# Kernel optimization log

Hardware: AMD Instinct MI355X
Metric: run time of the kernel (lower is better)

Reference implementation:

```python
import jax, jax.numpy as jnp
import numpy as np

B = 262144
HIST = 24
FORE = 20
HID = 256
# torch: tau_int = clamp(tau,1,18).long().item(); default tau=6.0 -> static 6 (host sync in torch)
TAU_INT = 6


def setup_inputs() -> dict:
    key = jax.random.key(0)
    ks = jax.random.split(key, 9)
    s = 0.1
    return {
        "history": jax.random.normal(ks[0], (B, HIST), jnp.float32),
        "enc_w1": jax.random.normal(ks[1], (HIST + FORE, HID), jnp.float32) * s,
        "enc_b1": jnp.zeros((HID,), jnp.float32),
        "enc_w2": jax.random.normal(ks[2], (HID, HID), jnp.float32) * s,
        "enc_b2": jnp.zeros((HID,), jnp.float32),
        "cor_w1": jax.random.normal(ks[3], (HID, HID), jnp.float32) * s,
        "cor_b1": jnp.zeros((HID,), jnp.float32),
        "cor_w2": jax.random.normal(ks[4], (HID, FORE), jnp.float32) * s,
        "cor_b2": jnp.zeros((FORE,), jnp.float32),
        "alpha": jnp.float32(0.2),
        "beta": jnp.float32(0.3),
        "gamma": jnp.float32(0.01),
        "tau": jnp.float32(6.0),
        "lambda_mix": jnp.float32(0.5),
    }


def _physics_core(history, alpha, beta, gamma, steps):
    a = jax.nn.sigmoid(alpha)
    b = jax.nn.sigmoid(beta)
    g = jnp.abs(gamma)
    T0 = history[:, -1]                      # [B]
    buf0 = history[:, -TAU_INT:].T           # [tau, B]; buf0[0] = history[:, -tau]

    def step(carry, _):
        T, buf = carry
        T_delayed = buf[0]
        T_new = T - a * T - b * T_delayed - g * T ** 3
        buf = jnp.concatenate([buf[1:], T_new[None, :]], axis=0)
        return (T_new, buf), T_new

    _, preds = jax.lax.scan(step, (T0, buf0), None, length=steps)
    return preds.T                            # [B, steps]


def reference(history, enc_w1, enc_b1, enc_w2, enc_b2,
              cor_w1, cor_b1, cor_w2, cor_b2,
              alpha, beta, gamma, tau, lambda_mix):
    T_physics = _physics_core(history, alpha, beta, gamma, FORE)   # [B, FORE]
    combined = jnp.concatenate([history, T_physics], axis=1)       # [B, HIST+FORE]
    h = jnp.tanh(combined @ enc_w1 + enc_b1)
    features = jnp.tanh(h @ enc_w2 + enc_b2)
    c = jnp.tanh(features @ cor_w1 + cor_b1)
    T_soft = c @ cor_w2 + cor_b2                                   # [B, FORE]
    lam = jax.nn.sigmoid(lambda_mix)
    T_pred = T_physics + lam * T_soft
    return (T_pred, T_physics, T_soft)
```

## Files before the change

### kernel.cpp

```cpp
#include <hip/hip_runtime.h>
#include <hip/hip_bf16.h>

#define NROWS 262144
#define HISTC 24
#define FOREC 20

typedef __bf16        v8bf __attribute__((ext_vector_type(8)));
typedef float         v4f  __attribute__((ext_vector_type(4)));
typedef float         v2f  __attribute__((ext_vector_type(2)));
typedef unsigned int  v4u  __attribute__((ext_vector_type(4)));
typedef unsigned int  v2u  __attribute__((ext_vector_type(2)));

#define WS_WT1_OFF 64
#define WT1_ELEMS 16384
#define WT2_ELEMS 65536
#define WT3_ELEMS 65536
#define WT4_ELEMS 8192

__device__ __forceinline__ unsigned short f2bf(float x) {
    unsigned u = __builtin_bit_cast(unsigned, x);
    u += 0x7FFFu + ((u >> 16) & 1u);
    return (unsigned short)(u >> 16);
}

__device__ __forceinline__ unsigned pack2bf(float a, float b) {
    unsigned ua = __builtin_bit_cast(unsigned, a);
    unsigned ub = __builtin_bit_cast(unsigned, b);
    ua += 0x7FFFu + ((ua >> 16) & 1u);
    ub += 0x7FFFu + ((ub >> 16) & 1u);
    return (ua >> 16) | (ub & 0xFFFF0000u);
}

__device__ __forceinline__ float fast_tanh(float x) {
    float t = x * 2.885390081777927f;
    float p = __builtin_amdgcn_exp2f(t);
    float r = __builtin_amdgcn_rcpf(p + 1.0f);
    return __builtin_fmaf(-2.0f, r, 1.0f);
}

__global__ void prep_kernel(const float* __restrict__ w1, const float* __restrict__ w2,
                            const float* __restrict__ w3, const float* __restrict__ w4,
                            const float* __restrict__ alpha, const float* __restrict__ beta,
                            const float* __restrict__ gamma, const float* __restrict__ lmix,
                            unsigned char* __restrict__ ws)
{
    if (blockIdx.x == 76) {
        int t = threadIdx.x;
        float* wsf = (float*)ws;
        if (t == 0) wsf[0] = 1.0f / (1.0f + expf(-alpha[0]));
        else if (t == 1) wsf[1] = 1.0f / (1.0f + expf(-beta[0]));
        else if (t == 2) wsf[2] = fabsf(gamma[0]);
        else if (t == 3) wsf[3] = 1.0f / (1.0f + expf(-lmix[0]));
        return;
    }
    int idx = (blockIdx.x * 256 + threadIdx.x) * 8;
    const float* src;
    int KT, Kreal, Nreal, srcN, local;
    unsigned short* dst = (unsigned short*)(ws + WS_WT1_OFF);
    if (idx < WT1_ELEMS) {
        local = idx; src = w1; KT = 2; Kreal = 44; Nreal = 256; srcN = 256;
    } else if (idx < WT1_ELEMS + WT2_ELEMS) {
        local = idx - WT1_ELEMS; dst += WT1_ELEMS;
        src = w2; KT = 8; Kreal = 256; Nreal = 256; srcN = 256;
    } else if (idx < WT1_ELEMS + WT2_ELEMS + WT3_ELEMS) {
        local = idx - (WT1_ELEMS + WT2_ELEMS); dst += WT1_ELEMS + WT2_ELEMS;
        src = w3; KT = 8; Kreal = 256; Nreal = 256; srcN = 256;
    } else {
        local = idx - (WT1_ELEMS + WT2_ELEMS + WT3_ELEMS);
        dst += WT1_ELEMS + WT2_ELEMS + WT3_ELEMS;
        src = w4; KT = 8; Kreal = 256; Nreal = 20; srcN = 20;
    }
    int L   = (local >> 3) & 63;
    int blk = local >> 9;
    int kt = blk % KT, nt = blk / KT;
    int cc = L & 15,  qq = L >> 4;
    int feat = nt * 16 + cc;
    int kbase = kt * 32 + qq * 8;
    unsigned short tmp[8];
#pragma unroll
    for (int j = 0; j < 8; ++j) {
        int k = kbase + j;
        float v = (k < Kreal && feat < Nreal) ? src[k * srcN + feat] : 0.0f;
        tmp[j] = f2bf(v);
    }
    v4u pk;
    pk[0] = tmp[0] | ((unsigned)tmp[1] << 16);
    pk[1] = tmp[2] | ((unsigned)tmp[3] << 16);
    pk[2] = tmp[4] | ((unsigned)tmp[5] << 16);
    pk[3] = tmp[6] | ((unsigned)tmp[7] << 16);
    *(v4u*)&dst[local] = pk;
}

template<int KT>
__device__ __forceinline__ void layer123(unsigned short* buf,
        const unsigned short* __restrict__ wsw, const float* __restrict__ bias,
        int w, int c, int q, int lane)
{
    const v4u* wp = (const v4u*)wsw;
    v4f acc[4][4];
#pragma unroll
    for (int ft = 0; ft < 4; ++ft)
#pragma unroll
        for (int st = 0; st < 4; ++st) {
            v4f z = {0.0f, 0.0f, 0.0f, 0.0f};
            acc[ft][st] = z;
        }

#pragma unroll 2
    for (int kt = 0; kt < KT; ++kt) {
        v4u a[4];
#pragma unroll
        for (int ft = 0; ft < 4; ++ft)
            a[ft] = wp[((w * 4 + ft) * KT + kt) * 64 + lane];
#pragma unroll
        for (int st = 0; st < 4; ++st) {
            v4u braw = *(const v4u*)&buf[(st * 16 + c) * 264 + kt * 32 + q * 8];
            v8bf bb = __builtin_bit_cast(v8bf, braw);
#pragma unroll
            for (int ft = 0; ft < 4; ++ft)
                acc[ft][st] = __builtin_amdgcn_mfma_f32_16x16x32_bf16(
                    __builtin_bit_cast(v8bf, a[ft]), bb, acc[ft][st], 0, 0, 0);
        }
    }

    __syncthreads();

#pragma unroll
    for (int ft = 0; ft < 4; ++ft) {
        v4f bi = *(const v4f*)&bias[w * 64 + ft * 16 + q * 4];
#pragma unroll
        for (int st = 0; st < 4; ++st) {
            float x0 = fast_tanh(acc[ft][st][0] + bi[0]);
            float x1 = fast_tanh(acc[ft][st][1] + bi[1]);
            float x2 = fast_tanh(acc[ft][st][2] + bi[2]);
            float x3 = fast_tanh(acc[ft][st][3] + bi[3]);
            v2u d; d[0] = pack2bf(x0, x1); d[1] = pack2bf(x2, x3);
            *(v2u*)&buf[(st * 16 + c) * 264 + w * 64 + ft * 16 + q * 4] = d;
        }
    }
    __syncthreads();
}

__global__ __launch_bounds__(256, 4) void fused_kernel(
    const float* __restrict__ history,
    const float* __restrict__ eb1, const float* __restrict__ eb2,
    const float* __restrict__ cb1, const float* __restrict__ cb2,
    const unsigned char* __restrict__ ws, float* __restrict__ out)
{
    __shared__ unsigned short buf[64 * 264];
    __shared__ float tp[64 * 20];

    const int tid  = threadIdx.x;
    const int w    = tid >> 6;
    const int lane = tid & 63;
    const int c    = lane & 15;
    const int q    = lane >> 4;
    const int row0 = blockIdx.x << 6;
    const float* wsf = (const float*)ws;
    const unsigned short* wt1 = (const unsigned short*)(ws + WS_WT1_OFF);
    const unsigned short* wt2 = wt1 + WT1_ELEMS;
    const unsigned short* wt3 = wt2 + WT2_ELEMS;
    const unsigned short* wt4 = wt3 + WT3_ELEMS;

#pragma unroll
    for (int i = 0; i < 2; ++i) {
        int e = tid + i * 256;
        if (e < 384) {
            int r  = e / 6, c4 = e - r * 6;
            v4f h4 = *(const v4f*)&history[(long)(row0 + r) * 24 + c4 * 4];
            v2u d; d[0] = pack2bf(h4[0], h4[1]); d[1] = pack2bf(h4[2], h4[3]);
            *(v2u*)&buf[r * 264 + c4 * 4] = d;
        }
    }
#pragma unroll
    for (int i = 0; i < 2; ++i) {
        int e = tid + i * 256;
        if (e < 320) {
            int r = e / 5, g = e - r * 5;
            v2u z = {0u, 0u};
            *(v2u*)&buf[r * 264 + 44 + g * 4] = z;
        }
    }
    if (tid < 64) {
        const float* hrow = &history[(long)(row0 + tid) * 24];
        v2f h18 = *(const v2f*)&hrow[18];
        v4f h20 = *(const v4f*)&hrow[20];
        float pa = wsf[0], pb = wsf[1], pg = wsf[2];
        float d0 = h18[0], d1 = h18[1], d2 = h20[0];
        float d3 = h20[1], d4 = h20[2], d5 = h20[3];
        float T = d5;
#pragma unroll
        for (int s = 0; s < 20; ++s) {
            float t3 = T * T * T;
            float Tn = T - pa * T;
            Tn = Tn - pb * d0;
            Tn = Tn - pg * t3;
            tp[tid * 20 + s] = Tn;
            buf[tid * 264 + 24 + s] = f2bf(Tn);
            d0 = d1; d1 = d2; d2 = d3; d3 = d4; d4 = d5; d5 = Tn;
            T = Tn;
        }
    }
    __syncthreads();

    layer123<2>(buf, wt1, eb1, w, c, q, lane);
    layer123<8>(buf, wt2, eb2, w, c, q, lane);
    layer123<8>(buf, wt3, cb1, w, c, q, lane);

    const v4u* wp4 = (const v4u*)wt4;
    v4f acc40 = {0.0f, 0.0f, 0.0f, 0.0f}, acc41 = {0.0f, 0.0f, 0.0f, 0.0f};
#pragma unroll 2
    for (int kt = 0; kt < 8; ++kt) {
        v4u a0 = wp4[(0 * 8 + kt) * 64 + lane];
        v4u a1 = wp4[(1 * 8 + kt) * 64 + lane];
        v4u braw = *(const v4u*)&buf[(w * 16 + c) * 264 + kt * 32 + q * 8];
        v8bf bb = __builtin_bit_cast(v8bf, braw);
        acc40 = __builtin_amdgcn_mfma_f32_16x16x32_bf16(
            __builtin_bit_cast(v8bf, a0), bb, acc40, 0, 0, 0);
        acc41 = __builtin_amdgcn_mfma_f32_16x16x32_bf16(
            __builtin_bit_cast(v8bf, a1), bb, acc41, 0, 0, 0);
    }

    const float lam = wsf[3];
    const long sample = (long)row0 + w * 16 + c;
    float* outP = out;
    float* outF = out + (long)NROWS * 20;
    float* outS = out + (long)NROWS * 40;
    {
        int f0 = q * 4;
        v4f bi  = *(const v4f*)&cb2[f0];
        v4f tph = *(const v4f*)&tp[(w * 16 + c) * 20 + f0];
        v4f ts, pr;
#pragma unroll
        for (int r = 0; r < 4; ++r) {
            ts[r] = acc40[r] + bi[r];
            pr[r] = tph[r] + lam * ts[r];
        }
        *(v4f*)&outS[sample * 20 + f0] = ts;
        *(v4f*)&outP[sample * 20 + f0] = pr;
        *(v4f*)&outF[sample * 20 + f0] = tph;
    }
    if (q == 0) {
        v4f bi  = *(const v4f*)&cb2[16];
        v4f tph = *(const v4f*)&tp[(w * 16 + c) * 20 + 16];
        v4f ts, pr;
#pragma unroll
        for (int r = 0; r < 4; ++r) {
            ts[r] = acc41[r] + bi[r];
            pr[r] = tph[r] + lam * ts[r];
        }
        *(v4f*)&outS[sample * 20 + 16] = ts;
        *(v4f*)&outP[sample * 20 + 16] = pr;
        *(v4f*)&outF[sample * 20 + 16] = tph;
    }
}

extern "C" void kernel_launch(void* const* d_in, const int* in_sizes, int n_in,
                              void* d_out, int out_size, void* d_ws, size_t ws_size,
                              hipStream_t stream)
{
    const float* history = (const float*)d_in[0];
    const float* enc_w1  = (const float*)d_in[1];
    const float* enc_b1  = (const float*)d_in[2];
    const float* enc_w2  = (const float*)d_in[3];
    const float* enc_b2  = (const float*)d_in[4];
    const float* cor_w1  = (const float*)d_in[5];
    const float* cor_b1  = (const float*)d_in[6];
    const float* cor_w2  = (const float*)d_in[7];
    const float* cor_b2  = (const float*)d_in[8];
    const float* alpha   = (const float*)d_in[9];
    const float* beta    = (const float*)d_in[10];
    const float* gamma   = (const float*)d_in[11];
    const float* lmix    = (const float*)d_in[13];

    prep_kernel<<<77, 256, 0, stream>>>(enc_w1, enc_w2, cor_w1, cor_w2,
                                        alpha, beta, gamma, lmix,
                                        (unsigned char*)d_ws);
    fused_kernel<<<NROWS / 64, 256, 0, stream>>>(history, enc_b1, enc_b2, cor_b1, cor_b2,
                                                 (const unsigned char*)d_ws, (float*)d_out);
}
```

Measured before the change: 210.9 us.

## Software-pipeline weight fragment loads across layers with a three-slot register ring

Replaces per-k-step weight loads with a triple-buffered register ring that prefetches weight fragments two k-steps ahead. The prefetch carries across layer boundaries, so the next layer's first tiles load during the current one. The last layer's weights are replicated per wave (the workspace grows), which lets each wave index its own copy in the prefetch. Launch bounds drop from 4 to 3 blocks per CU to make room for the extra registers, at the cost of occupancy.

```diff
diff --git a/kernel.cpp b/kernel.cpp
--- a/kernel.cpp
+++ b/kernel.cpp
@@ -15,7 +15,7 @@
 #define WT1_ELEMS 16384
 #define WT2_ELEMS 65536
 #define WT3_ELEMS 65536
-#define WT4_ELEMS 8192
+#define WT4R_ELEMS 65536
 
 __device__ __forceinline__ unsigned short f2bf(float x) {
     unsigned u = __builtin_bit_cast(unsigned, x);
@@ -23,7 +23,7 @@
     return (unsigned short)(u >> 16);
 }
 
-__device__ __forceinline__ unsigned pack2bf(float a, float b) {
+__device__ __forceinline__ unsigned packbf2(float a, float b) {
     unsigned ua = __builtin_bit_cast(unsigned, a);
     unsigned ub = __builtin_bit_cast(unsigned, b);
     ua += 0x7FFFu + ((ua >> 16) & 1u);
@@ -44,7 +44,7 @@
                             const float* __restrict__ gamma, const float* __restrict__ lmix,
                             unsigned char* __restrict__ ws)
 {
-    if (blockIdx.x == 76) {
+    if (blockIdx.x == 104) {
         int t = threadIdx.x;
         float* wsf = (float*)ws;
         if (t == 0) wsf[0] = 1.0f / (1.0f + expf(-alpha[0]));
@@ -55,24 +55,24 @@
     }
     int idx = (blockIdx.x * 256 + threadIdx.x) * 8;
     const float* src;
-    int KT, Kreal, Nreal, srcN, local;
+    int KT, Kreal, Nreal, srcN, local, ntmask;
     unsigned short* dst = (unsigned short*)(ws + WS_WT1_OFF);
     if (idx < WT1_ELEMS) {
-        local = idx; src = w1; KT = 2; Kreal = 44; Nreal = 256; srcN = 256;
+        local = idx; src = w1; KT = 2; Kreal = 44; Nreal = 256; srcN = 256; ntmask = 255;
     } else if (idx < WT1_ELEMS + WT2_ELEMS) {
         local = idx - WT1_ELEMS; dst += WT1_ELEMS;
-        src = w2; KT = 8; Kreal = 256; Nreal = 256; srcN = 256;
+        src = w2; KT = 8; Kreal = 256; Nreal = 256; srcN = 256; ntmask = 255;
     } else if (idx < WT1_ELEMS + WT2_ELEMS + WT3_ELEMS) {
         local = idx - (WT1_ELEMS + WT2_ELEMS); dst += WT1_ELEMS + WT2_ELEMS;
-        src = w3; KT = 8; Kreal = 256; Nreal = 256; srcN = 256;
+        src = w3; KT = 8; Kreal = 256; Nreal = 256; srcN = 256; ntmask = 255;
     } else {
         local = idx - (WT1_ELEMS + WT2_ELEMS + WT3_ELEMS);
         dst += WT1_ELEMS + WT2_ELEMS + WT3_ELEMS;
-        src = w4; KT = 8; Kreal = 256; Nreal = 20; srcN = 20;
+        src = w4; KT = 8; Kreal = 256; Nreal = 20; srcN = 20; ntmask = 1;
     }
     int L   = (local >> 3) & 63;
     int blk = local >> 9;
-    int kt = blk % KT, nt = blk / KT;
+    int kt = blk % KT, nt = (blk / KT) & ntmask;
     int cc = L & 15,  qq = L >> 4;
     int feat = nt * 16 + cc;
     int kbase = kt * 32 + qq * 8;
@@ -91,12 +91,12 @@
     *(v4u*)&dst[local] = pk;
 }
 
-template<int KT>
-__device__ __forceinline__ void layer123(unsigned short* buf,
-        const unsigned short* __restrict__ wsw, const float* __restrict__ bias,
+template<int KT, int KTN, int S0>
+__device__ __forceinline__ void layer_pipe(unsigned short* buf,
+        const v4u* __restrict__ wp, const v4u* __restrict__ wpn,
+        const float* __restrict__ bias, v4u A[3][4],
         int w, int c, int q, int lane)
 {
-    const v4u* wp = (const v4u*)wsw;
     v4f acc[4][4];
 #pragma unroll
     for (int ft = 0; ft < 4; ++ft)
@@ -106,12 +106,19 @@
             acc[ft][st] = z;
         }
 
-#pragma unroll 2
+#pragma unroll
     for (int kt = 0; kt < KT; ++kt) {
-        v4u a[4];
-#pragma unroll
-        for (int ft = 0; ft < 4; ++ft)
-            a[ft] = wp[((w * 4 + ft) * KT + kt) * 64 + lane];
+        const int cs = (S0 + kt) % 3;
+        const int ps = (S0 + kt + 2) % 3;
+        if (kt + 2 < KT) {
+#pragma unroll
+            for (int ft = 0; ft < 4; ++ft)
+                A[ps][ft] = wp[((w * 4 + ft) * KT + kt + 2) * 64 + lane];
+        } else {
+#pragma unroll
+            for (int ft = 0; ft < 4; ++ft)
+                A[ps][ft] = wpn[((w * 4 + ft) * KTN + (kt + 2 - KT)) * 64 + lane];
+        }
 #pragma unroll
         for (int st = 0; st < 4; ++st) {
             v4u braw = *(const v4u*)&buf[(st * 16 + c) * 264 + kt * 32 + q * 8];
@@ -119,7 +126,7 @@
 #pragma unroll
             for (int ft = 0; ft < 4; ++ft)
                 acc[ft][st] = __builtin_amdgcn_mfma_f32_16x16x32_bf16(
-                    __builtin_bit_cast(v8bf, a[ft]), bb, acc[ft][st], 0, 0, 0);
+                    __builtin_bit_cast(v8bf, A[cs][ft]), bb, acc[ft][st], 0, 0, 0);
         }
     }
 
@@ -134,14 +141,14 @@
             float x1 = fast_tanh(acc[ft][st][1] + bi[1]);
             float x2 = fast_tanh(acc[ft][st][2] + bi[2]);
             float x3 = fast_tanh(acc[ft][st][3] + bi[3]);
-            v2u d; d[0] = pack2bf(x0, x1); d[1] = pack2bf(x2, x3);
+            v2u d; d[0] = packbf2(x0, x1); d[1] = packbf2(x2, x3);
             *(v2u*)&buf[(st * 16 + c) * 264 + w * 64 + ft * 16 + q * 4] = d;
         }
     }
     __syncthreads();
 }
 
-__global__ __launch_bounds__(256, 4) void fused_kernel(
+__global__ __launch_bounds__(256, 3) void fused_kernel(
     const float* __restrict__ history,
     const float* __restrict__ eb1, const float* __restrict__ eb2,
     const float* __restrict__ cb1, const float* __restrict__ cb2,
@@ -157,10 +164,17 @@
     const int q    = lane >> 4;
     const int row0 = blockIdx.x << 6;
     const float* wsf = (const float*)ws;
-    const unsigned short* wt1 = (const unsigned short*)(ws + WS_WT1_OFF);
-    const unsigned short* wt2 = wt1 + WT1_ELEMS;
-    const unsigned short* wt3 = wt2 + WT2_ELEMS;
-    const unsigned short* wt4 = wt3 + WT3_ELEMS;
+    const v4u* wp1 = (const v4u*)(ws + WS_WT1_OFF);
+    const v4u* wp2 = wp1 + WT1_ELEMS / 8;
+    const v4u* wp3 = wp2 + WT2_ELEMS / 8;
+    const v4u* wp4 = wp3 + WT3_ELEMS / 8;
+
+    v4u A[3][4];
+#pragma unroll
+    for (int ft = 0; ft < 4; ++ft) {
+        A[0][ft] = wp1[((w * 4 + ft) * 2 + 0) * 64 + lane];
+        A[1][ft] = wp1[((w * 4 + ft) * 2 + 1) * 64 + lane];
+    }
 
 #pragma unroll
     for (int i = 0; i < 2; ++i) {
@@ -168,7 +182,7 @@
         if (e < 384) {
             int r  = e / 6, c4 = e - r * 6;
             v4f h4 = *(const v4f*)&history[(long)(row0 + r) * 24 + c4 * 4];
-            v2u d; d[0] = pack2bf(h4[0], h4[1]); d[1] = pack2bf(h4[2], h4[3]);
+            v2u d; d[0] = packbf2(h4[0], h4[1]); d[1] = packbf2(h4[2], h4[3]);
             *(v2u*)&buf[r * 264 + c4 * 4] = d;
         }
     }
@@ -203,22 +217,24 @@
     }
     __syncthreads();
 
-    layer123<2>(buf, wt1, eb1, w, c, q, lane);
-    layer123<8>(buf, wt2, eb2, w, c, q, lane);
-    layer123<8>(buf, wt3, cb1, w, c, q, lane);
-
-    const v4u* wp4 = (const v4u*)wt4;
+    layer_pipe<2, 8, 0>(buf, wp1, wp2, eb1, A, w, c, q, lane);
+    layer_pipe<8, 8, 2>(buf, wp2, wp3, eb2, A, w, c, q, lane);
+    layer_pipe<8, 8, 1>(buf, wp3, wp4, cb1, A, w, c, q, lane);
+
     v4f acc40 = {0.0f, 0.0f, 0.0f, 0.0f}, acc41 = {0.0f, 0.0f, 0.0f, 0.0f};
-#pragma unroll 2
+#pragma unroll
     for (int kt = 0; kt < 8; ++kt) {
-        v4u a0 = wp4[(0 * 8 + kt) * 64 + lane];
-        v4u a1 = wp4[(1 * 8 + kt) * 64 + lane];
+        const int cs = kt % 3, ps = (kt + 2) % 3;
+        if (kt + 2 < 8) {
+            A[ps][0] = wp4[((w * 4 + 0) * 8 + kt + 2) * 64 + lane];
+            A[ps][1] = wp4[((w * 4 + 1) * 8 + kt + 2) * 64 + lane];
+        }
         v4u braw = *(const v4u*)&buf[(w * 16 + c) * 264 + kt * 32 + q * 8];
         v8bf bb = __builtin_bit_cast(v8bf, braw);
         acc40 = __builtin_amdgcn_mfma_f32_16x16x32_bf16(
-            __builtin_bit_cast(v8bf, a0), bb, acc40, 0, 0, 0);
+            __builtin_bit_cast(v8bf, A[cs][0]), bb, acc40, 0, 0, 0);
         acc41 = __builtin_amdgcn_mfma_f32_16x16x32_bf16(
-            __builtin_bit_cast(v8bf, a1), bb, acc41, 0, 0, 0);
+            __builtin_bit_cast(v8bf, A[cs][1]), bb, acc41, 0, 0, 0);
     }
 
     const float lam = wsf[3];
@@ -273,9 +289,9 @@
     const float* gamma   = (const float*)d_in[11];
     const float* lmix    = (const float*)d_in[13];
 
-    prep_kernel<<<77, 256, 0, stream>>>(enc_w1, enc_w2, cor_w1, cor_w2,
-                                        alpha, beta, gamma, lmix,
-                                        (unsigned char*)d_ws);
+    prep_kernel<<<105, 256, 0, stream>>>(enc_w1, enc_w2, cor_w1, cor_w2,
+                                         alpha, beta, gamma, lmix,
+                                         (unsigned char*)d_ws);
     fused_kernel<<<NROWS / 64, 256, 0, stream>>>(history, enc_b1, enc_b2, cor_b1, cor_b2,
                                                  (const unsigned char*)d_ws, (float*)d_out);
 }
```

After: 207.3 us. No clear change (-1.7%).
